# Kernel tuning notes

Hardware: AMD Instinct MI355X
Metric: run time of the kernel (lower is better)

Reference implementation:

```python
import jax, jax.numpy as jnp
import numpy as np


def _procrustes_align(X, Y):
    """Batched similarity-transform (scipy-style Procrustes, reflection allowed).
    Aligns Y (pred) to X (target). X, Y: [B, N, 3]. Returns aligned Y: [B, N, 3].
    """
    muX = X.mean(axis=1, keepdims=True)                      # [B,1,3]
    muY = Y.mean(axis=1, keepdims=True)
    X0 = X - muX
    Y0 = Y - muY
    normX = jnp.sqrt((X0 ** 2).sum(axis=(1, 2), keepdims=True))  # [B,1,1]
    normY = jnp.sqrt((Y0 ** 2).sum(axis=(1, 2), keepdims=True))
    X0n = X0 / normX
    Y0n = Y0 / normY
    # 3x3 cross-covariance per batch element
    M = jnp.einsum('bni,bnj->bij', X0n, Y0n)                 # [B,3,3]
    U, s, Vt = jnp.linalg.svd(M)                             # batched tiny SVD
    # Optimal rotation Q = V @ U^T = (U @ Vt)^T  (minimizes ||Y0n @ Q - X0n||)
    Q = jnp.swapaxes(jnp.matmul(U, Vt), -1, -2)              # [B,3,3]
    traceTA = s.sum(-1)[:, None, None]                       # [B,1,1]
    Z = normX * traceTA * jnp.einsum('bni,bij->bnj', Y0n, Q) + muX
    return Z


def setup_inputs() -> dict:
    key = jax.random.key(0)
    k1, k2 = jax.random.split(key)
    B, N = 262144, 21
    pred_kp3d = jax.random.normal(k1, (B, N, 3), dtype=jnp.float32)
    target_kp3d = jax.random.normal(k2, (B, N, 3), dtype=jnp.float32)
    return {"pred_kp3d": pred_kp3d, "target_kp3d": target_kp3d}


def reference(pred_kp3d, target_kp3d):
    pred_aligned = _procrustes_align(target_kp3d, pred_kp3d)
    # mean per-joint Euclidean distance (PA-MPJPE style)
    err = jnp.sqrt(((pred_aligned - target_kp3d) ** 2).sum(-1)).mean()
    return err
```

## Files before the change

kernel.cpp:

```cpp
#include <hip/hip_runtime.h>
#include <math.h>

#define NPTS 21
#define FLB  63
#define CB   32
#define BPW  (2 * CB)
#define THREADS 64
#define TVEC (CB * FLB / 4)
#define TAILL 56
#define KMAX 11

#define SBAR() __builtin_amdgcn_sched_barrier(0)

#define LOAD8(v, g) do { \
    v##0 = (g)[0*64+lane]; v##1 = (g)[1*64+lane]; v##2 = (g)[2*64+lane]; \
    v##3 = (g)[3*64+lane]; v##4 = (g)[4*64+lane]; v##5 = (g)[5*64+lane]; \
    v##6 = (g)[6*64+lane]; if (lane < TAILL) v##7 = (g)[7*64+lane]; } while(0)

#define STORE8(v) do { \
    w4[0*64+lane] = v##0; w4[1*64+lane] = v##1; w4[2*64+lane] = v##2; \
    w4[3*64+lane] = v##3; w4[4*64+lane] = v##4; w4[5*64+lane] = v##5; \
    w4[6*64+lane] = v##6; if (lane < TAILL) w4[7*64+lane] = v##7; } while(0)

#define PASSA() do { \
    sy0=0.f; sy1=0.f; sy2=0.f; syy=0.f; \
    _Pragma("unroll") \
    for (int k = 0; k < KMAX; ++k) { \
        const int n = 2*k + sub; \
        if (n < NPTS) { \
            const int o = base + 3*n; \
            float a = sb[o+0], e = sb[o+1], c = sb[o+2]; \
            py0[k]=a; py1[k]=e; py2[k]=c; \
            sy0+=a; sy1+=e; sy2+=c; \
            syy = fmaf(a,a,fmaf(e,e,fmaf(c,c,syy))); \
        } else { py0[k]=0.f; py1[k]=0.f; py2[k]=0.f; } \
    } } while(0)

#define COMB(v) { v += __shfl_xor(v, 32, 64); }

#define PASSB() do { \
    float sx0=0.f, sx1=0.f, sx2=0.f; \
    float m00=0,m01=0,m02=0, m10=0,m11=0,m12=0, m20=0,m21=0,m22=0; \
    _Pragma("unroll") \
    for (int k = 0; k < KMAX; ++k) { \
        const int n = 2*k + sub; \
        if (n < NPTS) { \
            const int o = base + 3*n; \
            float u = sb[o+0], v = sb[o+1], x2 = sb[o+2]; \
            float a = py0[k], e = py1[k], c = py2[k]; \
            sx0+=u; sx1+=v; sx2+=x2; \
            m00=fmaf(u,a,m00); m01=fmaf(u,e,m01); m02=fmaf(u,c,m02); \
            m10=fmaf(v,a,m10); m11=fmaf(v,e,m11); m12=fmaf(v,c,m12); \
            m20=fmaf(x2,a,m20); m21=fmaf(x2,e,m21); m22=fmaf(x2,c,m22); \
        } \
    } \
    COMB(sy0) COMB(sy1) COMB(sy2) COMB(syy) \
    COMB(sx0) COMB(sx1) COMB(sx2) \
    COMB(m00) COMB(m01) COMB(m02) \
    COMB(m10) COMB(m11) COMB(m12) \
    COMB(m20) COMB(m21) COMB(m22) \
    const float invN = 1.0f / (float)NPTS; \
    float mux0=sx0*invN, mux1=sx1*invN, mux2=sx2*invN; \
    float muy0=sy0*invN, muy1=sy1*invN, muy2=sy2*invN; \
    float ny2 = syy - (sy0*sy0 + sy1*sy1 + sy2*sy2) * invN; \
    float c00=m00-sx0*sy0*invN, c01=m01-sx0*sy1*invN, c02=m02-sx0*sy2*invN; \
    float c10=m10-sx1*sy0*invN, c11=m11-sx1*sy1*invN, c12=m12-sx1*sy2*invN; \
    float c20=m20-sx2*sy0*invN, c21=m21-sx2*sy1*invN, c22=m22-sx2*sy2*invN; \
    float q00=c00, q01=c10, q02=c20, \
          q10=c01, q11=c11, q12=c21, \
          q20=c02, q21=c12, q22=c22; \
    _Pragma("unroll") \
    for (int it = 0; it < 6; ++it) { \
        float C00=q11*q22-q12*q21, C01=q12*q20-q10*q22, C02=q10*q21-q11*q20; \
        float C10=q02*q21-q01*q22, C11=q00*q22-q02*q20, C12=q01*q20-q00*q21; \
        float C20=q01*q12-q02*q11, C21=q02*q10-q00*q12, C22=q00*q11-q01*q10; \
        float det = q00*C00 + q01*C01 + q02*C02; \
        float ad  = fmaxf(fabsf(det), 1e-30f); \
        float sdet = copysignf(ad, det); \
        float g  = __expf(0.333333333f * __logf(ad)); \
        float ha = 0.5f / g; \
        float hb = 0.5f * g / sdet; \
        q00=ha*q00+hb*C00; q01=ha*q01+hb*C01; q02=ha*q02+hb*C02; \
        q10=ha*q10+hb*C10; q11=ha*q11+hb*C11; q12=ha*q12+hb*C12; \
        q20=ha*q20+hb*C20; q21=ha*q21+hb*C21; q22=ha*q22+hb*C22; \
    } \
    float trP = q00*c00 + q01*c10 + q02*c20 \
              + q10*c01 + q11*c11 + q12*c21 \
              + q20*c02 + q21*c12 + q22*c22; \
    float kk = trP / ny2; \
    float r00=kk*q00, r01=kk*q01, r02=kk*q02; \
    float r10=kk*q10, r11=kk*q11, r12=kk*q12; \
    float r20=kk*q20, r21=kk*q21, r22=kk*q22; \
    _Pragma("unroll") \
    for (int k = 0; k < KMAX; ++k) { \
        const int n = 2*k + sub; \
        if (n < NPTS) { \
            const int o = base + 3*n; \
            float xa = sb[o+0], xb = sb[o+1], xc = sb[o+2]; \
            float u = py0[k]-muy0, v = py1[k]-muy1, x2 = py2[k]-muy2; \
            float z0 = fmaf(u,r00,fmaf(v,r10,fmaf(x2,r20,mux0))) - xa; \
            float z1 = fmaf(u,r01,fmaf(v,r11,fmaf(x2,r21,mux1))) - xb; \
            float z2 = fmaf(u,r02,fmaf(v,r12,fmaf(x2,r22,mux2))) - xc; \
            errsum += sqrtf(fmaf(z0,z0,fmaf(z1,z1,z2*z2))); \
        } \
    } } while(0)

__global__ __launch_bounds__(THREADS, 3)
void pa_mpjpe(const float* __restrict__ pred,
              const float* __restrict__ targ,
              float* __restrict__ ws,
              int B)
{
    __shared__ __align__(16) float sb[CB * FLB];
    float4* w4 = (float4*)sb;

    const int lane = threadIdx.x & 63;
    const int b    = lane & (CB - 1);
    const int sub  = (lane >> 5) & 1;
    const int base = b * FLB;
    const int b0   = blockIdx.x * BPW;

    const float4* gp0 = (const float4*)(pred + (size_t)b0 * FLB);
    const float4* gt0 = (const float4*)(targ + (size_t)b0 * FLB);
    const float4* gp1 = gp0 + TVEC;
    const float4* gt1 = gt0 + TVEC;

    float4 rp0, rp1, rp2, rp3, rp4, rp5, rp6, rp7 = make_float4(0,0,0,0);
    float4 rt0, rt1, rt2, rt3, rt4, rt5, rt6, rt7 = make_float4(0,0,0,0);
    float py0[KMAX], py1[KMAX], py2[KMAX];
    float sy0, sy1, sy2, syy;
    float errsum = 0.0f;

    LOAD8(rp, gp0);
    LOAD8(rt, gt0);
    SBAR();
    STORE8(rp);
    SBAR();
    LOAD8(rp, gp1);
    SBAR();
    PASSA();
    SBAR();
    STORE8(rt);
    SBAR();
    LOAD8(rt, gt1);
    SBAR();
    PASSB();
    SBAR();
    STORE8(rp);
    SBAR();
    PASSA();
    SBAR();
    STORE8(rt);
    SBAR();
    PASSB();

    #pragma unroll
    for (int off = 32; off > 0; off >>= 1) errsum += __shfl_down(errsum, off, 64);
    if (lane == 0) ws[blockIdx.x] = errsum;
}

__global__ __launch_bounds__(256)
void pa_reduce(const float* __restrict__ ws, float* __restrict__ out,
               int nblk, float inv_total)
{
    __shared__ float sw[4];
    float s = 0.0f;
    const float4* w4 = (const float4*)ws;
    const int n4 = nblk >> 2;
    for (int i = threadIdx.x; i < n4; i += 256) {
        float4 v = w4[i];
        s += (v.x + v.y) + (v.z + v.w);
    }
    #pragma unroll
    for (int off = 32; off > 0; off >>= 1) s += __shfl_down(s, off, 64);
    if ((threadIdx.x & 63) == 0) sw[threadIdx.x >> 6] = s;
    __syncthreads();
    if (threadIdx.x == 0)
        out[0] = (sw[0] + sw[1] + sw[2] + sw[3]) * inv_total;
}

extern "C" void kernel_launch(void* const* d_in, const int* in_sizes, int n_in,
                              void* d_out, int out_size, void* d_ws, size_t ws_size,
                              hipStream_t stream)
{
    const float* pred = (const float*)d_in[0];
    const float* targ = (const float*)d_in[1];
    float* out = (float*)d_out;
    float* ws  = (float*)d_ws;

    int B = in_sizes[0] / FLB;
    int grid = (B + BPW - 1) / BPW;
    float inv_total = 1.0f / ((float)B * (float)NPTS);

    pa_mpjpe<<<grid, THREADS, 0, stream>>>(pred, targ, ws, B);
    pa_reduce<<<1, 256, 0, stream>>>(ws, out, grid, inv_total);
}
```

Before: 154.7 us.

## Use persistent grid with four chunks per block and prefetch next chunk

Changes from one block per 64 batch elements to a fixed grid of 2048 single-wave blocks. Each block loops over four 32-element chunks strided by the grid size, and the next chunk's global loads are issued before the current chunk's SVD/error pass. This is meant to cut block launch overhead and overlap memory latency with compute. The grid is hardcoded, so it only covers B=262144 (2048*4*32) and silently assumes that size; it also reduces the number of waves in flight.

Result: faster. 150.1 us (-3.0%).

```diff
diff --git a/kernel.cpp b/kernel.cpp
--- a/kernel.cpp
+++ b/kernel.cpp
@@ -4,11 +4,11 @@
 #define NPTS 21
 #define FLB  63
 #define CB   32
-#define BPW  (2 * CB)
 #define THREADS 64
 #define TVEC (CB * FLB / 4)
 #define TAILL 56
 #define KMAX 11
+#define GRID 2048
 
 #define SBAR() __builtin_amdgcn_sched_barrier(0)
 
@@ -118,12 +118,6 @@
     const int b    = lane & (CB - 1);
     const int sub  = (lane >> 5) & 1;
     const int base = b * FLB;
-    const int b0   = blockIdx.x * BPW;
-
-    const float4* gp0 = (const float4*)(pred + (size_t)b0 * FLB);
-    const float4* gt0 = (const float4*)(targ + (size_t)b0 * FLB);
-    const float4* gp1 = gp0 + TVEC;
-    const float4* gt1 = gt0 + TVEC;
 
     float4 rp0, rp1, rp2, rp3, rp4, rp5, rp6, rp7 = make_float4(0,0,0,0);
     float4 rt0, rt1, rt2, rt3, rt4, rt5, rt6, rt7 = make_float4(0,0,0,0);
@@ -131,28 +125,33 @@
     float sy0, sy1, sy2, syy;
     float errsum = 0.0f;
 
-    LOAD8(rp, gp0);
-    LOAD8(rt, gt0);
+    {
+        const float4* gp = (const float4*)(pred + (size_t)blockIdx.x * (CB*FLB));
+        const float4* gt = (const float4*)(targ + (size_t)blockIdx.x * (CB*FLB));
+        LOAD8(rp, gp);
+        LOAD8(rt, gt);
+    }
     SBAR();
-    STORE8(rp);
-    SBAR();
-    LOAD8(rp, gp1);
-    SBAR();
-    PASSA();
-    SBAR();
-    STORE8(rt);
-    SBAR();
-    LOAD8(rt, gt1);
-    SBAR();
-    PASSB();
-    SBAR();
-    STORE8(rp);
-    SBAR();
-    PASSA();
-    SBAR();
-    STORE8(rt);
-    SBAR();
-    PASSB();
+
+    #pragma unroll
+    for (int i = 0; i < 4; ++i) {
+        STORE8(rp);
+        SBAR();
+        PASSA();
+        SBAR();
+        STORE8(rt);
+        SBAR();
+        if (i < 3) {
+            const size_t c = (size_t)blockIdx.x + (size_t)(i + 1) * GRID;
+            const float4* gp = (const float4*)(pred + c * (CB*FLB));
+            const float4* gt = (const float4*)(targ + c * (CB*FLB));
+            LOAD8(rp, gp);
+            LOAD8(rt, gt);
+            SBAR();
+        }
+        PASSB();
+        SBAR();
+    }
 
     #pragma unroll
     for (int off = 32; off > 0; off >>= 1) errsum += __shfl_down(errsum, off, 64);
@@ -189,7 +188,7 @@
     float* ws  = (float*)d_ws;
 
     int B = in_sizes[0] / FLB;
-    int grid = (B + BPW - 1) / BPW;
+    int grid = GRID;
     float inv_total = 1.0f / ((float)B * (float)NPTS);
 
     pa_mpjpe<<<grid, THREADS, 0, stream>>>(pred, targ, ws, B);
```
